# Kernel tuning notes

Measured on AMD Instinct MI355X. Metric: run time of the kernel, lower is better.

## Reference

```python
import jax, jax.numpy as jnp
import numpy as np

N = 100000   # nodes
E = 3200000  # edges
M = 4096     # moves
K = 16       # orders per move
NEG_SLOPE = 0.2  # PyG GATv2Conv default negative_slope

PARAM_SHAPES = {
    'g1_Wl': (10, 15), 'g1_Wr': (10, 15), 'g1_att': (10,), 'g1_b': (10,),
    'g2_Wl': (10, 25), 'g2_Wr': (10, 25), 'g2_att': (10,), 'g2_b': (10,),
    'g3_Wl': (10, 25), 'g3_Wr': (10, 25), 'g3_att': (10,), 'g3_b': (10,),
    'vt_W': (20, 29), 'vt_b': (20,), 'va_W': (1, 20), 'va_b': (1,),
    'vv_W': (10, 20), 'vv_b': (10,), 'vl_W': (1, 10), 'vl_b': (1,),
    'at_W': (20, 48), 'at_b': (20,), 'dt_W': (20, 23), 'dt_b': (20,),
    'oa_W': (1, 20), 'oa_b': (1,), 'ov_W': (1, 20), 'ov_b': (1,),
}
PARAM_NAMES = list(PARAM_SHAPES.keys())


def _linear(x, W, b):
    return x @ W.T + b


def _gatv2(x, src, dst, Wl, Wr, att, b):
    # GATv2Conv (heads=1, self-loops appended by caller), eval mode (no dropout)
    xl = x @ Wl.T  # messages from source nodes
    xr = x @ Wr.T
    e = (jax.nn.leaky_relu(xl[src] + xr[dst], NEG_SLOPE) * att).sum(-1)  # [E+N]
    emax = jax.ops.segment_max(e, dst, num_segments=N)
    ee = jnp.exp(e - emax[dst])
    denom = jax.ops.segment_sum(ee, dst, num_segments=N)
    alpha = ee / denom[dst]
    return jax.ops.segment_sum(alpha[:, None] * xl[src], dst, num_segments=N) + b


def _forward(x1, x2, edges, move_src, move_dst, move_armies, is_attack, params):
    (g1_Wl, g1_Wr, g1_att, g1_b,
     g2_Wl, g2_Wr, g2_att, g2_b,
     g3_Wl, g3_Wr, g3_att, g3_b,
     vt_W, vt_b, va_W, va_b, vv_W, vv_b, vl_W, vl_b,
     at_W, at_b, dt_W, dt_b, oa_W, oa_b, ov_W, ov_b) = params
    x2t = jnp.tile(x2, (N, 1))  # [N,4]
    self_idx = jnp.arange(N, dtype=edges.dtype)
    src = jnp.concatenate([edges[0], self_idx])
    dst = jnp.concatenate([edges[1], self_idx])
    x = jax.nn.relu(_gatv2(x1, src, dst, g1_Wl, g1_Wr, g1_att, g1_b))
    x = jax.nn.relu(_gatv2(jnp.concatenate([x, x1], 1), src, dst, g2_Wl, g2_Wr, g2_att, g2_b))
    x = jax.nn.relu(_gatv2(jnp.concatenate([x, x1], 1), src, dst, g3_Wl, g3_Wr, g3_att, g3_b))  # [N,10]
    # per-move order tensors (vectorized over [M,K]); deploy uses move_src as target
    xs, xd = x[move_src], x[move_dst]       # [M,K,10]
    x1s, x1d = x1[move_src], x1[move_dst]   # [M,K,15]
    extra = 0.6 * move_armies - 0.7 * (x1d[..., 3] + x1d[..., 4])
    attack_in = jnp.concatenate([xs, xd, x1s[..., 3:], x1d[..., 1:],
                                 move_armies[..., None], extra[..., None]], -1)  # [M,K,48]
    deploy_in = jnp.concatenate([xs, x1s[..., 3:], move_armies[..., None]], -1)  # [M,K,23]
    feat = jnp.where(is_attack[..., None] == 1,
                     _linear(attack_in, at_W, at_b),
                     _linear(deploy_in, dt_W, dt_b))
    feat = jax.nn.relu(feat)  # dropout = identity (eval)
    attn = jax.nn.softmax(_linear(feat, oa_W, oa_b), axis=1)  # softmax over orders
    p = (attn * _linear(feat, ov_W, ov_b)).sum(axis=(1, 2))   # [M]
    # value head: attention pooling over all nodes
    Vn = jax.nn.relu(_linear(jnp.concatenate([x, x1, x2t], 1), vt_W, vt_b))  # [N,20]
    vatt = jax.nn.softmax(_linear(Vn, va_W, va_b), axis=0)
    Vp = jax.nn.relu((vatt * _linear(Vn, vv_W, vv_b)).sum(axis=0))
    V = jnp.tanh(_linear(Vp, vl_W, vl_b))[0]
    return V, jax.nn.log_softmax(p, axis=0)


def setup_inputs() -> dict:
    key = jax.random.key(0)
    ks = iter(jax.random.split(key, 64))
    inp = {
        'x1': jax.random.normal(next(ks), (N, 15), jnp.float32),
        'x2': jax.random.normal(next(ks), (4,), jnp.float32),
        'edges': jax.random.randint(next(ks), (2, E), 0, N, jnp.int32),
        'move_src': jax.random.randint(next(ks), (M, K), 0, N, jnp.int32),
        'move_dst': jax.random.randint(next(ks), (M, K), 0, N, jnp.int32),
        'move_armies': jax.random.uniform(next(ks), (M, K), jnp.float32) * 10.0,
        'is_attack': jax.random.randint(next(ks), (M, K), 0, 2, jnp.int32),
    }
    for name, shape in PARAM_SHAPES.items():
        inp[name] = jax.random.normal(next(ks), shape, jnp.float32) * 0.1
    return inp


def reference(x1, x2, edges, move_src, move_dst, move_armies, is_attack,
              g1_Wl, g1_Wr, g1_att, g1_b, g2_Wl, g2_Wr, g2_att, g2_b,
              g3_Wl, g3_Wr, g3_att, g3_b, vt_W, vt_b, va_W, va_b,
              vv_W, vv_b, vl_W, vl_b, at_W, at_b, dt_W, dt_b,
              oa_W, oa_b, ov_W, ov_b):
    params = (g1_Wl, g1_Wr, g1_att, g1_b, g2_Wl, g2_Wr, g2_att, g2_b,
              g3_Wl, g3_Wr, g3_att, g3_b, vt_W, vt_b, va_W, va_b,
              vv_W, vv_b, vl_W, vl_b, at_W, at_b, dt_W, dt_b,
              oa_W, oa_b, ov_W, ov_b)
    return _forward(x1, x2, edges, move_src, move_dst, move_armies, is_attack, params)
```

## Files before the change

kernel.cpp:

```cpp
#include <hip/hip_runtime.h>
#include <hip/hip_fp16.h>
#include <math.h>

#define NN 100000
#define NE 3200000
#define MM 4096
#define KK 16
#define NEG_SLOPE 0.2f
#define SUB 8
#define BSH 8
#define NB 391
#define PCH 4096
#define FCAP 9728
#define XS 12
#define XSU 4
#define PART_BLOCKS ((NE + NN + PCH - 1) / PCH)
#define LIN_BLOCKS  ((NN + 1023) / 1024)
#define MOVE_BLOCKS ((MM * KK) / 256)
#define VAL_BLOCKS  ((NN + 255) / 256)
#define PZ ((int)0xAAAAAAAAu)

typedef float vfloat2 __attribute__((__vector_size__(2 * sizeof(float))));

__device__ __forceinline__ void f8x10_decode(const uint4& w, float* xs) {
    vfloat2 f0 = __builtin_amdgcn_cvt_pk_f32_fp8(w.x, false); xs[0]=f0[0]; xs[1]=f0[1];
    vfloat2 f1 = __builtin_amdgcn_cvt_pk_f32_fp8(w.x, true);  xs[2]=f1[0]; xs[3]=f1[1];
    vfloat2 f2 = __builtin_amdgcn_cvt_pk_f32_fp8(w.y, false); xs[4]=f2[0]; xs[5]=f2[1];
    vfloat2 f3 = __builtin_amdgcn_cvt_pk_f32_fp8(w.y, true);  xs[6]=f3[0]; xs[7]=f3[1];
    vfloat2 f4 = __builtin_amdgcn_cvt_pk_f32_fp8(w.z, false); xs[8]=f4[0]; xs[9]=f4[1];
}
__device__ __forceinline__ uint4 f8x10_encode(const float* v) {
    unsigned u0 = __builtin_amdgcn_cvt_pk_fp8_f32(v[0], v[1], 0, false);
    u0 = __builtin_amdgcn_cvt_pk_fp8_f32(v[2], v[3], u0, true);
    unsigned u1 = __builtin_amdgcn_cvt_pk_fp8_f32(v[4], v[5], 0, false);
    u1 = __builtin_amdgcn_cvt_pk_fp8_f32(v[6], v[7], u1, true);
    unsigned u2 = __builtin_amdgcn_cvt_pk_fp8_f32(v[8], v[9], 0, false);
    return make_uint4(u0, u1, u2, 0u);
}

__global__ __launch_bounds__(1024) void part_lin1_kernel(const int* __restrict__ edges,
                                                         int* __restrict__ cnt,
                                                         unsigned* __restrict__ recs,
                                                         const float* __restrict__ x1,
                                                         const float* __restrict__ Wl,
                                                         const float* __restrict__ Wr,
                                                         unsigned* __restrict__ xl8,
                                                         float* __restrict__ xr) {
    int t = threadIdx.x;
    if (blockIdx.x >= PART_BLOCKS) {
        int i = (blockIdx.x - PART_BLOCKS) * 1024 + t;
        if (i >= NN) return;
        float in[15];
        #pragma unroll
        for (int j = 0; j < 15; j++) in[j] = x1[(long)i * 15 + j];
        float sl[10];
        #pragma unroll
        for (int o = 0; o < 10; o++) {
            float l = 0.f, r = 0.f;
            #pragma unroll
            for (int j = 0; j < 15; j++) {
                l += Wl[o * 15 + j] * in[j];
                r += Wr[o * 15 + j] * in[j];
            }
            sl[o] = l;
            xr[(long)i * XS + o] = r;
        }
        *(uint4*)(xl8 + (long)i * XSU) = f8x10_encode(sl);
        return;
    }
    __shared__ unsigned rl[PCH];
    __shared__ unsigned short bb[PCH];
    __shared__ int h[NB];
    __shared__ int gb[NB];
    __shared__ int cur[NB];
    const int total = NE + NN;
    int base = blockIdx.x * PCH;
    int n = min(PCH, total - base);
    if (t < NB) { h[t] = 0; cur[t] = 0; }
    __syncthreads();
    for (int j = t; j < n; j += 1024) {
        int i = base + j;
        int s, d;
        if (i < NE) { s = edges[i]; d = edges[NE + i]; }
        else        { s = i - NE; d = s; }
        rl[j] = ((unsigned)(d & 255) << 17) | (unsigned)s;
        int b = d >> BSH;
        bb[j] = (unsigned short)b;
        atomicAdd(&h[b], 1);
    }
    __syncthreads();
    if (t < NB) {
        int hv = h[t];
        if (hv > 0) gb[t] = atomicAdd(&cnt[t], hv) - PZ;
    }
    __syncthreads();
    for (int j = t; j < n; j += 1024) {
        int b = bb[j];
        int l = atomicAdd(&cur[b], 1);
        int pos = gb[b] + l;
        if (pos >= 0 && pos < FCAP) recs[(long)b * FCAP + pos] = rl[j];
    }
}

__global__ __launch_bounds__(1024) void fine_sort_kernel(const unsigned* __restrict__ recs,
                                                         const int* __restrict__ cnt,
                                                         int* __restrict__ csr_src,
                                                         int* __restrict__ offsets) {
    __shared__ unsigned rl[FCAP];
    __shared__ int scn[512];
    __shared__ int hist[256];
    __shared__ int sc[256];
    __shared__ int hb[257];
    __shared__ int cur[256];
    int b = blockIdx.x;
    int t = threadIdx.x;
    int c = 0;
    if (t < 512) {
        c = (t < NB) ? min(max(cnt[t] - PZ, 0), FCAP) : 0;
        scn[t] = c;
    }
    __syncthreads();
    for (int off = 1; off < 512; off <<= 1) {
        int v = 0;
        if (t < 512 && t >= off) v = scn[t - off];
        __syncthreads();
        if (t < 512) scn[t] += v;
        __syncthreads();
    }
    int beg = (b == 0) ? 0 : scn[b - 1];
    int nb = min(max(cnt[b] - PZ, 0), FCAP);
    int nodebase = b << BSH;
    int nnodes = min(256, NN - nodebase);
    if (t < 256) { hist[t] = 0; cur[t] = 0; }
    __syncthreads();
    const unsigned* rsrc = recs + (long)b * FCAP;
    for (int j = t; j < nb; j += 1024) {
        unsigned r = rsrc[j];
        rl[j] = r;
        atomicAdd(&hist[r >> 17], 1);
    }
    __syncthreads();
    int hv = (t < 256) ? hist[t] : 0;
    if (t < 256) sc[t] = hv;
    __syncthreads();
    for (int off = 1; off < 256; off <<= 1) {
        int v = 0;
        if (t < 256 && t >= off) v = sc[t - off];
        __syncthreads();
        if (t < 256) sc[t] += v;
        __syncthreads();
    }
    if (t < 256) hb[t] = sc[t] - hv;
    if (t == 0) hb[256] = nb;
    __syncthreads();
    for (int j = t; j < nb; j += 1024) {
        unsigned r = rl[j];
        int l = r >> 17;
        int p = hb[l] + atomicAdd(&cur[l], 1);
        csr_src[beg + p] = (int)(r & 0x1FFFFu);
    }
    if (t < nnodes) offsets[nodebase + t] = beg + hb[t];
    if (b == NB - 1 && t == 0) offsets[NN] = beg + nb;
}

template<bool FUSE_NEXT>
__global__ void gat_aggregate_kernel(const int* __restrict__ csr_src,
                                     const int* __restrict__ offsets,
                                     const unsigned* __restrict__ xl8,
                                     const float* __restrict__ xr,
                                     const float* __restrict__ att,
                                     const float* __restrict__ b,
                                     const float* __restrict__ x1,
                                     const float* __restrict__ nWl,
                                     const float* __restrict__ nWr,
                                     unsigned* __restrict__ xlo,
                                     float* __restrict__ xro,
                                     float* __restrict__ xout)
{
    int t = blockIdx.x * blockDim.x + threadIdx.x;
    int node = t / SUB;
    int lane = t % SUB;
    if (node >= NN) return;
    float xrn[12], a[10];
    const float4* xr4 = (const float4*)(xr + (long)node * XS);
    #pragma unroll
    for (int q = 0; q < 3; q++) {
        float4 v = xr4[q];
        xrn[4*q] = v.x; xrn[4*q+1] = v.y; xrn[4*q+2] = v.z; xrn[4*q+3] = v.w;
    }
    #pragma unroll
    for (int h = 0; h < 10; h++) a[h] = att[h];
    int beg = offsets[node], end = offsets[node + 1];
    float den = 0.f, num[10];
    #pragma unroll
    for (int h = 0; h < 10; h++) num[h] = 0.f;
    int j = beg + lane;
    for (; j + 3 * SUB < end; j += 4 * SUB) {
        int s0 = csr_src[j];
        int s1 = csr_src[j + SUB];
        int s2 = csr_src[j + 2 * SUB];
        int s3 = csr_src[j + 3 * SUB];
        uint4 wa[4];
        wa[0] = *(const uint4*)(xl8 + (long)s0 * XSU);
        wa[1] = *(const uint4*)(xl8 + (long)s1 * XSU);
        wa[2] = *(const uint4*)(xl8 + (long)s2 * XSU);
        wa[3] = *(const uint4*)(xl8 + (long)s3 * XSU);
        #pragma unroll
        for (int q = 0; q < 4; q++) {
            float xs[10];
            f8x10_decode(wa[q], xs);
            float e = 0.f;
            #pragma unroll
            for (int h = 0; h < 10; h++) {
                float v = xs[h] + xrn[h];
                v = (v >= 0.f) ? v : NEG_SLOPE * v;
                e += v * a[h];
            }
            float w = __expf(e);
            den += w;
            #pragma unroll
            for (int h = 0; h < 10; h++) num[h] += w * xs[h];
        }
    }
    for (; j < end; j += SUB) {
        int s = csr_src[j];
        uint4 wa = *(const uint4*)(xl8 + (long)s * XSU);
        float xs[10];
        f8x10_decode(wa, xs);
        float e = 0.f;
        #pragma unroll
        for (int h = 0; h < 10; h++) {
            float v = xs[h] + xrn[h];
            v = (v >= 0.f) ? v : NEG_SLOPE * v;
            e += v * a[h];
        }
        float w = __expf(e);
        den += w;
        #pragma unroll
        for (int h = 0; h < 10; h++) num[h] += w * xs[h];
    }
    #pragma unroll
    for (int off = SUB / 2; off; off >>= 1) {
        den += __shfl_xor(den, off, SUB);
        #pragma unroll
        for (int h = 0; h < 10; h++) num[h] += __shfl_xor(num[h], off, SUB);
    }
    float inv = 1.f / den;
    float xo[10];
    #pragma unroll
    for (int h = 0; h < 10; h++) xo[h] = fmaxf(num[h] * inv + b[h], 0.f);
    if (FUSE_NEXT) {
        if (lane < 5) {
            float in2[25];
            #pragma unroll
            for (int h = 0; h < 10; h++) in2[h] = xo[h];
            #pragma unroll
            for (int h = 0; h < 15; h++) in2[10 + h] = x1[(long)node * 15 + h];
            int o0 = 2 * lane, o1 = 2 * lane + 1;
            float sl0 = 0.f, sl1 = 0.f, sr0 = 0.f, sr1 = 0.f;
            #pragma unroll
            for (int jj = 0; jj < 25; jj++) {
                sl0 += nWl[o0 * 25 + jj] * in2[jj];
                sl1 += nWl[o1 * 25 + jj] * in2[jj];
                sr0 += nWr[o0 * 25 + jj] * in2[jj];
                sr1 += nWr[o1 * 25 + jj] * in2[jj];
            }
            unsigned pk = __builtin_amdgcn_cvt_pk_fp8_f32(sl0, sl1, 0, false);
            ((unsigned short*)(xlo + (long)node * XSU))[lane] = (unsigned short)pk;
            *(float2*)(xro + (long)node * XS + o0) = make_float2(sr0, sr1);
        }
    } else {
        if (lane == 0) {
            #pragma unroll
            for (int h = 0; h < 10; h++) xout[(long)node * XS + h] = xo[h];
        }
    }
}

__global__ void move_value_kernel(const float* __restrict__ x,
                                  const float* __restrict__ x1,
                                  const float* __restrict__ x2,
                                  const int* __restrict__ msrc,
                                  const int* __restrict__ mdst,
                                  const float* __restrict__ armies,
                                  const int* __restrict__ isatk,
                                  const float* __restrict__ at_W, const float* __restrict__ at_b,
                                  const float* __restrict__ dt_W, const float* __restrict__ dt_b,
                                  const float* __restrict__ oa_W, const float* __restrict__ oa_b,
                                  const float* __restrict__ ov_W, const float* __restrict__ ov_b,
                                  const float* __restrict__ vt_W, const float* __restrict__ vt_b,
                                  const float* __restrict__ va_W, const float* __restrict__ va_b,
                                  const float* __restrict__ vv_W, const float* __restrict__ vv_b,
                                  float* __restrict__ p,
                                  float* __restrict__ partials) {
    if (blockIdx.x < MOVE_BLOCKS) {
        int t = blockIdx.x * 256 + threadIdx.x;
        int m = t >> 4;
        int k = t & 15;
        int s = msrc[t], d = mdst[t];
        float arm = armies[t];
        bool atk = (isatk[t] == 1);
        float xsrc[12];
        const float4* xs4 = (const float4*)(x + (long)s * XS);
        #pragma unroll
        for (int q = 0; q < 3; q++) {
            float4 v = xs4[q];
            xsrc[4*q]=v.x; xsrc[4*q+1]=v.y; xsrc[4*q+2]=v.z; xsrc[4*q+3]=v.w;
        }
        float feat[20];
        if (atk) {
            float in[48];
            #pragma unroll
            for (int h = 0; h < 10; h++) in[h] = xsrc[h];
            const float4* xd4 = (const float4*)(x + (long)d * XS);
            float xdst[12];
            #pragma unroll
            for (int q = 0; q < 3; q++) {
                float4 v = xd4[q];
                xdst[4*q]=v.x; xdst[4*q+1]=v.y; xdst[4*q+2]=v.z; xdst[4*q+3]=v.w;
            }
            #pragma unroll
            for (int h = 0; h < 10; h++) in[10 + h] = xdst[h];
            #pragma unroll
            for (int h = 0; h < 12; h++) in[20 + h] = x1[(long)s * 15 + 3 + h];
            #pragma unroll
            for (int h = 0; h < 14; h++) in[32 + h] = x1[(long)d * 15 + 1 + h];
            in[46] = arm;
            in[47] = 0.6f * arm - 0.7f * (x1[(long)d * 15 + 3] + x1[(long)d * 15 + 4]);
            #pragma unroll
            for (int o = 0; o < 20; o++) {
                float sum = at_b[o];
                #pragma unroll
                for (int j = 0; j < 48; j++) sum += at_W[o * 48 + j] * in[j];
                feat[o] = fmaxf(sum, 0.f);
            }
        } else {
            float in[23];
            #pragma unroll
            for (int h = 0; h < 10; h++) in[h] = xsrc[h];
            #pragma unroll
            for (int h = 0; h < 12; h++) in[10 + h] = x1[(long)s * 15 + 3 + h];
            in[22] = arm;
            #pragma unroll
            for (int o = 0; o < 20; o++) {
                float sum = dt_b[o];
                #pragma unroll
                for (int j = 0; j < 23; j++) sum += dt_W[o * 23 + j] * in[j];
                feat[o] = fmaxf(sum, 0.f);
            }
        }
        float oa = oa_b[0], ov = ov_b[0];
        #pragma unroll
        for (int j = 0; j < 20; j++) {
            oa += oa_W[j] * feat[j];
            ov += ov_W[j] * feat[j];
        }
        float mx = oa;
        #pragma unroll
        for (int off = 8; off; off >>= 1) mx = fmaxf(mx, __shfl_xor(mx, off, 16));
        float w = __expf(oa - mx);
        float nume = w * ov;
        float den = w;
        #pragma unroll
        for (int off = 8; off; off >>= 1) {
            nume += __shfl_xor(nume, off, 16);
            den  += __shfl_xor(den,  off, 16);
        }
        if (k == 0) p[m] = nume / den;
        return;
    }
    __shared__ float sm[4][11];
    int vb = blockIdx.x - MOVE_BLOCKS;
    int i = vb * 256 + threadIdx.x;
    float w = 0.f;
    float acc[10];
    #pragma unroll
    for (int h = 0; h < 10; h++) acc[h] = 0.f;
    if (i < NN) {
        float in[29];
        const float4* xi4 = (const float4*)(x + (long)i * XS);
        float xi[12];
        #pragma unroll
        for (int q = 0; q < 3; q++) {
            float4 v = xi4[q];
            xi[4*q]=v.x; xi[4*q+1]=v.y; xi[4*q+2]=v.z; xi[4*q+3]=v.w;
        }
        #pragma unroll
        for (int h = 0; h < 10; h++) in[h] = xi[h];
        #pragma unroll
        for (int h = 0; h < 15; h++) in[10 + h] = x1[(long)i * 15 + h];
        #pragma unroll
        for (int h = 0; h < 4; h++) in[25 + h] = x2[h];
        float Vn[20];
        #pragma unroll
        for (int o = 0; o < 20; o++) {
            float s = vt_b[o];
            #pragma unroll
            for (int j = 0; j < 29; j++) s += vt_W[o * 29 + j] * in[j];
            Vn[o] = fmaxf(s, 0.f);
        }
        float lg = va_b[0];
        #pragma unroll
        for (int j = 0; j < 20; j++) lg += va_W[j] * Vn[j];
        w = __expf(lg);
        #pragma unroll
        for (int o = 0; o < 10; o++) {
            float s = vv_b[o];
            #pragma unroll
            for (int j = 0; j < 20; j++) s += vv_W[o * 20 + j] * Vn[j];
            acc[o] = w * s;
        }
    }
    #pragma unroll
    for (int off = 32; off; off >>= 1) {
        w += __shfl_xor(w, off, 64);
        #pragma unroll
        for (int h = 0; h < 10; h++) acc[h] += __shfl_xor(acc[h], off, 64);
    }
    int wid = threadIdx.x >> 6;
    if ((threadIdx.x & 63) == 0) {
        #pragma unroll
        for (int h = 0; h < 10; h++) sm[wid][h] = acc[h];
        sm[wid][10] = w;
    }
    __syncthreads();
    if (threadIdx.x < 11) {
        int c = threadIdx.x;
        partials[(long)vb * 12 + c] = sm[0][c] + sm[1][c] + sm[2][c] + sm[3][c];
    }
}

__global__ void final_kernel(const float* __restrict__ p,
                             const float* __restrict__ partials,
                             const float* __restrict__ vl_W, const float* __restrict__ vl_b,
                             float* __restrict__ out) {
    if (blockIdx.x == 0) {
        __shared__ float sm[256];
        int tid = threadIdx.x;
        float mx = -INFINITY;
        for (int i = tid; i < MM; i += 256) mx = fmaxf(mx, p[i]);
        sm[tid] = mx; __syncthreads();
        for (int s = 128; s; s >>= 1) { if (tid < s) sm[tid] = fmaxf(sm[tid], sm[tid + s]); __syncthreads(); }
        mx = sm[0]; __syncthreads();
        float sum = 0.f;
        for (int i = tid; i < MM; i += 256) sum += expf(p[i] - mx);
        sm[tid] = sum; __syncthreads();
        for (int s = 128; s; s >>= 1) { if (tid < s) sm[tid] += sm[tid + s]; __syncthreads(); }
        float ls = mx + logf(sm[0]);
        for (int i = tid; i < MM; i += 256) out[1 + i] = p[i] - ls;
    } else if (threadIdx.x < 64) {
        int lane = threadIdx.x;
        float s[11];
        #pragma unroll
        for (int c = 0; c < 11; c++) s[c] = 0.f;
        for (int j = lane; j < VAL_BLOCKS; j += 64)
            #pragma unroll
            for (int c = 0; c < 11; c++) s[c] += partials[(long)j * 12 + c];
        #pragma unroll
        for (int off = 32; off; off >>= 1)
            #pragma unroll
            for (int c = 0; c < 11; c++) s[c] += __shfl_xor(s[c], off, 64);
        if (lane == 0) {
            float inv = 1.0f / s[10];
            float v = vl_b[0];
            #pragma unroll
            for (int h = 0; h < 10; h++) v += vl_W[h] * fmaxf(s[h] * inv, 0.f);
            out[0] = tanhf(v);
        }
    }
}

extern "C" void kernel_launch(void* const* d_in, const int* in_sizes, int n_in,
                              void* d_out, int out_size, void* d_ws, size_t ws_size,
                              hipStream_t stream) {
    const float* x1      = (const float*)d_in[0];
    const float* x2      = (const float*)d_in[1];
    const int*   edges   = (const int*)d_in[2];
    const int*   msrc    = (const int*)d_in[3];
    const int*   mdst    = (const int*)d_in[4];
    const float* armies  = (const float*)d_in[5];
    const int*   isatk   = (const int*)d_in[6];
    const float* g1_Wl = (const float*)d_in[7],  *g1_Wr = (const float*)d_in[8];
    const float* g1_att= (const float*)d_in[9],  *g1_b  = (const float*)d_in[10];
    const float* g2_Wl = (const float*)d_in[11], *g2_Wr = (const float*)d_in[12];
    const float* g2_att= (const float*)d_in[13], *g2_b  = (const float*)d_in[14];
    const float* g3_Wl = (const float*)d_in[15], *g3_Wr = (const float*)d_in[16];
    const float* g3_att= (const float*)d_in[17], *g3_b  = (const float*)d_in[18];
    const float* vt_W  = (const float*)d_in[19], *vt_b  = (const float*)d_in[20];
    const float* va_W  = (const float*)d_in[21], *va_b  = (const float*)d_in[22];
    const float* vv_W  = (const float*)d_in[23], *vv_b  = (const float*)d_in[24];
    const float* vl_W  = (const float*)d_in[25], *vl_b  = (const float*)d_in[26];
    const float* at_W  = (const float*)d_in[27], *at_b  = (const float*)d_in[28];
    const float* dt_W  = (const float*)d_in[29], *dt_b  = (const float*)d_in[30];
    const float* oa_W  = (const float*)d_in[31], *oa_b  = (const float*)d_in[32];
    const float* ov_W  = (const float*)d_in[33], *ov_b  = (const float*)d_in[34];

    float* out = (float*)d_out;

    float* ws = (float*)d_ws;
    unsigned* xl8A = (unsigned*)ws;
    unsigned* xl8B = xl8A + (long)NN * XSU;
    float* xrA = (float*)(xl8B + (long)NN * XSU);
    float* xrB = xrA + (long)NN * XS;
    float* xF  = xrB + (long)NN * XS;
    int* csr_src = (int*)(xF + (long)NN * XS);
    int* offsets = csr_src + (NE + NN);
    unsigned* recs = (unsigned*)(offsets + NN + 4);
    int* cnt   = (int*)(recs + (long)NB * FCAP);
    float* pbuf = (float*)(cnt + NB + 1);
    float* partials = pbuf + MM;

    const int aggBlocks = ((long)NN * SUB + 255) / 256;

    part_lin1_kernel<<<PART_BLOCKS + LIN_BLOCKS, 1024, 0, stream>>>(
        edges, cnt, recs, x1, g1_Wl, g1_Wr, xl8A, xrA);
    fine_sort_kernel<<<NB, 1024, 0, stream>>>(recs, cnt, csr_src, offsets);
    gat_aggregate_kernel<true><<<aggBlocks, 256, 0, stream>>>(
        csr_src, offsets, xl8A, xrA, g1_att, g1_b, x1, g2_Wl, g2_Wr, xl8B, xrB, nullptr);
    gat_aggregate_kernel<true><<<aggBlocks, 256, 0, stream>>>(
        csr_src, offsets, xl8B, xrB, g2_att, g2_b, x1, g3_Wl, g3_Wr, xl8A, xrA, nullptr);
    gat_aggregate_kernel<false><<<aggBlocks, 256, 0, stream>>>(
        csr_src, offsets, xl8A, xrA, g3_att, g3_b, x1, nullptr, nullptr, nullptr, nullptr, xF);
    move_value_kernel<<<MOVE_BLOCKS + VAL_BLOCKS, 256, 0, stream>>>(
        xF, x1, x2, msrc, mdst, armies, isatk,
        at_W, at_b, dt_W, dt_b, oa_W, oa_b, ov_W, ov_b,
        vt_W, vt_b, va_W, va_b, vv_W, vv_b, pbuf, partials);
    final_kernel<<<2, 256, 0, stream>>>(pbuf, partials, vl_W, vl_b, out);
}
```

Before: 330.4 us.

## Shrink partition blocks to 256 threads, hold records in registers, pad bucket counters

```diff
diff --git a/kernel.cpp b/kernel.cpp
--- a/kernel.cpp
+++ b/kernel.cpp
@@ -15,9 +15,11 @@
 #define XS 12
 #define XSU 4
 #define PART_BLOCKS ((NE + NN + PCH - 1) / PCH)
-#define LIN_BLOCKS  ((NN + 1023) / 1024)
+#define LIN_BLOCKS  ((NN + 255) / 256)
 #define MOVE_BLOCKS ((MM * KK) / 256)
 #define VAL_BLOCKS  ((NN + 255) / 256)
+#define RPT (PCH / 256)
+#define CSTR 16
 #define PZ ((int)0xAAAAAAAAu)
 
 typedef float vfloat2 __attribute__((__vector_size__(2 * sizeof(float))));
@@ -38,17 +40,17 @@
     return make_uint4(u0, u1, u2, 0u);
 }
 
-__global__ __launch_bounds__(1024) void part_lin1_kernel(const int* __restrict__ edges,
-                                                         int* __restrict__ cnt,
-                                                         unsigned* __restrict__ recs,
-                                                         const float* __restrict__ x1,
-                                                         const float* __restrict__ Wl,
-                                                         const float* __restrict__ Wr,
-                                                         unsigned* __restrict__ xl8,
-                                                         float* __restrict__ xr) {
+__global__ __launch_bounds__(256) void part_lin1_kernel(const int* __restrict__ edges,
+                                                        int* __restrict__ cnt,
+                                                        unsigned* __restrict__ recs,
+                                                        const float* __restrict__ x1,
+                                                        const float* __restrict__ Wl,
+                                                        const float* __restrict__ Wr,
+                                                        unsigned* __restrict__ xl8,
+                                                        float* __restrict__ xr) {
     int t = threadIdx.x;
     if (blockIdx.x >= PART_BLOCKS) {
-        int i = (blockIdx.x - PART_BLOCKS) * 1024 + t;
+        int i = (blockIdx.x - PART_BLOCKS) * 256 + t;
         if (i >= NN) return;
         float in[15];
         #pragma unroll
@@ -68,37 +70,44 @@
         *(uint4*)(xl8 + (long)i * XSU) = f8x10_encode(sl);
         return;
     }
-    __shared__ unsigned rl[PCH];
-    __shared__ unsigned short bb[PCH];
     __shared__ int h[NB];
     __shared__ int gb[NB];
     __shared__ int cur[NB];
     const int total = NE + NN;
     int base = blockIdx.x * PCH;
     int n = min(PCH, total - base);
-    if (t < NB) { h[t] = 0; cur[t] = 0; }
-    __syncthreads();
-    for (int j = t; j < n; j += 1024) {
-        int i = base + j;
-        int s, d;
-        if (i < NE) { s = edges[i]; d = edges[NE + i]; }
-        else        { s = i - NE; d = s; }
-        rl[j] = ((unsigned)(d & 255) << 17) | (unsigned)s;
-        int b = d >> BSH;
-        bb[j] = (unsigned short)b;
-        atomicAdd(&h[b], 1);
-    }
-    __syncthreads();
-    if (t < NB) {
-        int hv = h[t];
-        if (hv > 0) gb[t] = atomicAdd(&cnt[t], hv) - PZ;
-    }
-    __syncthreads();
-    for (int j = t; j < n; j += 1024) {
-        int b = bb[j];
-        int l = atomicAdd(&cur[b], 1);
-        int pos = gb[b] + l;
-        if (pos >= 0 && pos < FCAP) recs[(long)b * FCAP + pos] = rl[j];
+    for (int b = t; b < NB; b += 256) { h[b] = 0; cur[b] = 0; }
+    __syncthreads();
+    unsigned rrec[RPT];
+    int rbk[RPT];
+    #pragma unroll
+    for (int q = 0; q < RPT; q++) {
+        int j = t + q * 256;
+        rbk[q] = -1;
+        if (j < n) {
+            int i = base + j;
+            int s, d;
+            if (i < NE) { s = edges[i]; d = edges[NE + i]; }
+            else        { s = i - NE; d = s; }
+            rrec[q] = ((unsigned)(d & 255) << 17) | (unsigned)s;
+            int b = d >> BSH;
+            rbk[q] = b;
+            atomicAdd(&h[b], 1);
+        }
+    }
+    __syncthreads();
+    for (int b = t; b < NB; b += 256) {
+        int hv = h[b];
+        if (hv > 0) gb[b] = atomicAdd(&cnt[b * CSTR], hv) - PZ;
+    }
+    __syncthreads();
+    #pragma unroll
+    for (int q = 0; q < RPT; q++) {
+        int b = rbk[q];
+        if (b >= 0) {
+            int pos = gb[b] + atomicAdd(&cur[b], 1);
+            if (pos >= 0 && pos < FCAP) recs[(long)b * FCAP + pos] = rrec[q];
+        }
     }
 }
 
@@ -116,7 +125,7 @@
     int t = threadIdx.x;
     int c = 0;
     if (t < 512) {
-        c = (t < NB) ? min(max(cnt[t] - PZ, 0), FCAP) : 0;
+        c = (t < NB) ? min(max(cnt[t * CSTR] - PZ, 0), FCAP) : 0;
         scn[t] = c;
     }
     __syncthreads();
@@ -128,7 +137,7 @@
         __syncthreads();
     }
     int beg = (b == 0) ? 0 : scn[b - 1];
-    int nb = min(max(cnt[b] - PZ, 0), FCAP);
+    int nb = min(max(cnt[b * CSTR] - PZ, 0), FCAP);
     int nodebase = b << BSH;
     int nnodes = min(256, NN - nodebase);
     if (t < 256) { hist[t] = 0; cur[t] = 0; }
@@ -507,12 +516,12 @@
     int* offsets = csr_src + (NE + NN);
     unsigned* recs = (unsigned*)(offsets + NN + 4);
     int* cnt   = (int*)(recs + (long)NB * FCAP);
-    float* pbuf = (float*)(cnt + NB + 1);
+    float* pbuf = (float*)(cnt + NB * CSTR + 16);
     float* partials = pbuf + MM;
 
     const int aggBlocks = ((long)NN * SUB + 255) / 256;
 
-    part_lin1_kernel<<<PART_BLOCKS + LIN_BLOCKS, 1024, 0, stream>>>(
+    part_lin1_kernel<<<PART_BLOCKS + LIN_BLOCKS, 256, 0, stream>>>(
         edges, cnt, recs, x1, g1_Wl, g1_Wr, xl8A, xrA);
     fine_sort_kernel<<<NB, 1024, 0, stream>>>(recs, cnt, csr_src, offsets);
     gat_aggregate_kernel<true><<<aggBlocks, 256, 0, stream>>>(
```

Measured after the change: 334.5 us. Within noise of the previous version (+1.2%).
